# Performance work log

Measured on AMD Instinct MI355X. Metric: run time of the kernel, lower is better.

## Reference

```python
import jax, jax.numpy as jnp
import numpy as np

N, P, F, R, M = 20000, 320000, 128, 64, 32
F4 = F // 4            # n_atombasis // 4 == graph_n_messagebasis
L1 = 2                 # max_multipole_order + 1 (charges + dipoles)
N_BLOCKS = 2


def _w(key, fan_in, fan_out):
    return jax.random.normal(key, (fan_in, fan_out), dtype=jnp.float32) / np.sqrt(fan_in)


def setup_inputs() -> dict:
    key = jax.random.key(0)
    ks = jax.random.split(key, 24)
    inp = {
        'features': jax.random.normal(ks[0], (N, F), dtype=jnp.float32),
        'distances': jax.random.uniform(ks[1], (P,), dtype=jnp.float32),
        'vectors': jax.random.normal(ks[2], (P, 3), dtype=jnp.float32),
        'cutoffs': jax.random.uniform(ks[3], (P,), dtype=jnp.float32),
        'rbfs': jax.random.normal(ks[4], (P, R), dtype=jnp.float32),
        'idx_i': jnp.sort(jax.random.randint(ks[5], (P,), 0, N)),
        'idx_j': jax.random.randint(ks[6], (P,), 0, N),
    }
    d_inv = 6 * F4 + 2 * F   # (n_features_anisotropic+1)*(F//4) + 2*F = 448
    d_eq0 = F4 + 2 * F       # 288
    inp['Wrbf'] = _w(ks[7], R + 2 * F, F4)
    inp['Wemb'] = _w(ks[8], F, F)
    inp['eq0_W1'] = _w(ks[9], d_eq0, F)
    inp['eq0_b1'] = jnp.zeros((F,), jnp.float32)
    inp['eq0_W2'] = _w(ks[10], F, M * L1) * 0.01
    inp['eq1_W1'] = _w(ks[11], d_inv, F)
    inp['eq1_b1'] = jnp.zeros((F,), jnp.float32)
    inp['eq1_W2'] = _w(ks[12], F, M * L1) * 0.01
    inp['inv_W1'] = jnp.stack([_w(ks[13 + b], d_inv, F) for b in range(N_BLOCKS)])
    inp['inv_b1'] = jnp.zeros((N_BLOCKS, F), jnp.float32)
    inp['inv_W2'] = jnp.stack([_w(ks[15 + b], F, F) * 0.01 for b in range(N_BLOCKS)])
    inp['inv_b2'] = jnp.zeros((N_BLOCKS, F), jnp.float32)
    inp['upd_W1'] = jnp.stack([_w(ks[17 + b], 2 * F, F) for b in range(N_BLOCKS)])
    inp['upd_b1'] = jnp.zeros((N_BLOCKS, F), jnp.float32)
    inp['upd_W2'] = jnp.stack([_w(ks[19 + b], F, F) * 0.01 for b in range(N_BLOCKS)])
    inp['upd_b2'] = jnp.zeros((N_BLOCKS, F), jnp.float32)
    return inp


def reference(features, distances, vectors, cutoffs, rbfs, idx_i, idx_j,
              Wrbf, Wemb, eq0_W1, eq0_b1, eq0_W2, eq1_W1, eq1_b1, eq1_W2,
              inv_W1, inv_b1, inv_W2, inv_b2,
              upd_W1, upd_b1, upd_W2, upd_b2):
    silu = jax.nn.silu
    n_atoms = features.shape[0]
    # unit pair vectors (eps guards uniform distances near 0)
    u = vectors / (distances + 1e-3)[:, None]                 # [P,3]
    s = features                                              # [N,F] scalar features
    v = jnp.zeros((n_atoms, 3, M), dtype=features.dtype)      # [N,3,M] vector (dipole) features
    eq_params = [(eq0_W1, eq0_b1, eq0_W2), (eq1_W1, eq1_b1, eq1_W2)]
    for b in range(N_BLOCKS):
        si, sj = s[idx_i], s[idx_j]                           # gathers [P,F]
        e = jnp.concatenate([rbfs, si, sj], axis=-1) @ Wrbf   # pair embedding [P,F4]
        vi, vj = v[idx_i], v[idx_j]                           # [P,3,M]
        # anisotropic invariants of the equivariant features (5 of them, each [P,M])
        a_ui = jnp.einsum('pd,pdm->pm', u, vi)
        a_uj = jnp.einsum('pd,pdm->pm', u, vj)
        a_ij = jnp.sum(vi * vj, axis=1)
        a_ii = jnp.sum(vi * vi, axis=1)
        a_jj = jnp.sum(vj * vj, axis=1)
        x_inv = jnp.concatenate([e, a_ui, a_uj, a_ij, a_ii, a_jj, si, sj], axis=-1)  # [P,448]
        x_eq = jnp.concatenate([e, si, sj], axis=-1) if b == 0 else x_inv
        W1, b1, W2 = eq_params[b]
        g = silu(x_eq @ W1 + b1) @ W2                          # [P, M*2]
        g0, g1 = g[:, :M], g[:, M:]
        # equivariant message: radial direction term + propagated vector term
        dv = (g0[:, None, :] * u[:, :, None] + g1[:, None, :] * vj) * cutoffs[:, None, None]
        v = v + jax.ops.segment_sum(dv, idx_i, num_segments=n_atoms)
        # invariant message
        m = silu(silu(x_inv @ inv_W1[b] + inv_b1[b]) @ inv_W2[b] + inv_b2[b]) * cutoffs[:, None]
        s = s + jax.ops.segment_sum(m, idx_i, num_segments=n_atoms)
        # atom-wise update
        femb = s @ Wemb
        h = jnp.concatenate([s, femb], axis=-1)
        s = s + silu(silu(h @ upd_W1[b] + upd_b1[b]) @ upd_W2[b] + upd_b2[b])
    return s, v
```

## Files before the change

### kernel.cpp

```cpp
#include <hip/hip_runtime.h>
#include <math.h>

#define NA   20000
#define PE   320000
#define FDIM 128
#define ET   64
#define AT   32

typedef unsigned short ushort_t;
typedef __attribute__((ext_vector_type(8))) short bf16x8;
typedef __attribute__((ext_vector_type(4))) float f32x4;
#define MFMA16 __builtin_amdgcn_mfma_f32_16x16x32_bf16

#define XSTR     456
#define HSTR     136
#define XS_OFF   0
#define H1_OFF   58368
#define US_OFF   75776
#define IIS_OFF  76800
#define JJS_OFF  77064
#define SMEM_SZ  77320
#define ML_OFF   0
#define GL_OFF   33792

#define PK_W1EQ0   0
#define PK_W1EQ1   7168
#define PK_W1INV0  14336
#define PK_W1INV1  21504
#define PK_W2EQ0   28672
#define PK_W2EQ1   29696
#define PK_W2INV0  30720
#define PK_W2INV1  32768
#define PK_WRBF    34816
#define PK_WEMB    36096
#define PK_W1U0    38144
#define PK_W1U1    42240
#define PK_W2U0    46336
#define PK_W2U1    48384
#define PK_TOTAL   50432

__device__ __forceinline__ float silu_f(float z) {
    return z / (1.0f + __expf(-z));
}

__device__ __forceinline__ ushort_t f2bf(float x) {
    __bf16 h = (__bf16)x;
    union { __bf16 b; ushort_t u; } c; c.b = h; return c.u;
}

__device__ __forceinline__ unsigned int pack2bf(float x, float y) {
    return (unsigned int)f2bf(x) | ((unsigned int)f2bf(y) << 16);
}

__device__ __forceinline__ uint4 cvt8(float4 a, float4 b) {
    uint4 r;
    r.x = pack2bf(a.x, a.y); r.y = pack2bf(a.z, a.w);
    r.z = pack2bf(b.x, b.y); r.w = pack2bf(b.z, b.w);
    return r;
}

__global__ void pack_all(const float* __restrict__ eq0W1, const float* __restrict__ eq1W1,
                         const float* __restrict__ invW1, const float* __restrict__ eq0W2,
                         const float* __restrict__ eq1W2, const float* __restrict__ invW2,
                         const float* __restrict__ Wrbf,  const float* __restrict__ Wemb,
                         const float* __restrict__ updW1, const float* __restrict__ updW2,
                         ushort_t* __restrict__ out)
{
    const int tid = blockIdx.x * blockDim.x + threadIdx.x;
    if (tid >= PK_TOTAL) return;
    int base, KB, N, mode = 0;
    const float* src;
    if      (tid < PK_W1EQ1)  { base = PK_W1EQ0;  KB = 14; N = 128; src = eq0W1; mode = 1; }
    else if (tid < PK_W1INV0) { base = PK_W1EQ1;  KB = 14; N = 128; src = eq1W1; }
    else if (tid < PK_W1INV1) { base = PK_W1INV0; KB = 14; N = 128; src = invW1; }
    else if (tid < PK_W2EQ0)  { base = PK_W1INV1; KB = 14; N = 128; src = invW1 + 448 * 128; }
    else if (tid < PK_W2EQ1)  { base = PK_W2EQ0;  KB = 4;  N = 64;  src = eq0W2; }
    else if (tid < PK_W2INV0) { base = PK_W2EQ1;  KB = 4;  N = 64;  src = eq1W2; }
    else if (tid < PK_W2INV1) { base = PK_W2INV0; KB = 4;  N = 128; src = invW2; }
    else if (tid < PK_WRBF)   { base = PK_W2INV1; KB = 4;  N = 128; src = invW2 + 128 * 128; }
    else if (tid < PK_WEMB)   { base = PK_WRBF;   KB = 10; N = 32;  src = Wrbf; }
    else if (tid < PK_W1U0)   { base = PK_WEMB;   KB = 4;  N = 128; src = Wemb; }
    else if (tid < PK_W1U1)   { base = PK_W1U0;   KB = 8;  N = 128; src = updW1; }
    else if (tid < PK_W2U0)   { base = PK_W1U1;   KB = 8;  N = 128; src = updW1 + 256 * 128; }
    else if (tid < PK_W2U1)   { base = PK_W2U0;   KB = 4;  N = 128; src = updW2; }
    else                      { base = PK_W2U1;   KB = 4;  N = 128; src = updW2 + 128 * 128; }
    const int local = tid - base;
    const int lane  = local & 63;
    const int rest  = local >> 6;
    const int kb    = rest % KB;
    const int ct    = rest / KB;
    const int col   = ct * 16 + (lane & 15);
    const int k0    = kb * 32 + ((lane >> 4) * 8);
    ushort_t v[8];
    #pragma unroll
    for (int j = 0; j < 8; j++) {
        const int k = k0 + j;
        float x;
        if (mode == 1) x = (k < 32) ? src[k * N + col] : (k < 192 ? 0.f : src[(k - 160) * N + col]);
        else           x = src[(size_t)k * N + col];
        v[j] = f2bf(x);
    }
    *(uint4*)(out + (size_t)tid * 8) = *(uint4*)v;
}

__global__ __launch_bounds__(512, 4)
void edge_kernel(const float* __restrict__ rbfs,
                 const float* __restrict__ dists,
                 const float* __restrict__ vecs,
                 const float* __restrict__ cuts,
                 const int*   __restrict__ gidx_i,
                 const int*   __restrict__ gidx_j,
                 const ushort_t* __restrict__ s_bf,
                 const float* __restrict__ v_in,
                 const ushort_t* __restrict__ pWrbf,
                 const ushort_t* __restrict__ pW1eq,
                 const float* __restrict__ b1eq,
                 const ushort_t* __restrict__ pW2eq,
                 const ushort_t* __restrict__ pW1inv,
                 const float* __restrict__ b1inv,
                 const ushort_t* __restrict__ pW2inv,
                 const float* __restrict__ b2inv,
                 float* __restrict__ s_out,
                 float* __restrict__ v_out,
                 const int eqSkip)
{
    __shared__ __align__(16) char smem[SMEM_SZ];
    ushort_t* xs  = (ushort_t*)(smem + XS_OFF);
    ushort_t* h1  = (ushort_t*)(smem + H1_OFF);
    float*    us  = (float*)(smem + US_OFF);
    int*      iis = (int*)(smem + IIS_OFF);
    int*      jjs = (int*)(smem + JJS_OFF);
    float*    ml  = (float*)(smem + ML_OFF);
    float*    gl  = (float*)(smem + GL_OFF);

    const int t    = threadIdx.x;
    const int p0   = blockIdx.x * ET;
    const int lane = t & 63;
    const int wid  = t >> 6;
    const int colf = lane & 15;
    const int krow = (lane >> 4) * 8;

    {
        const int e = t >> 3, l = t & 7;
        const int p = p0 + e;
        const int i = gidx_i[p];
        const int j = gidx_j[p];
        const uint4* si4 = (const uint4*)(s_bf + (size_t)i * FDIM);
        const uint4* sj4 = (const uint4*)(s_bf + (size_t)j * FDIM);
        *(uint4*)&xs[e * XSTR + 192 + l * 16]     = si4[l * 2];
        *(uint4*)&xs[e * XSTR + 192 + l * 16 + 8] = si4[l * 2 + 1];
        *(uint4*)&xs[e * XSTR + 320 + l * 16]     = sj4[l * 2];
        *(uint4*)&xs[e * XSTR + 320 + l * 16 + 8] = sj4[l * 2 + 1];
        const float4* rb4 = (const float4*)(rbfs + (size_t)p * 64);
        float4 r0 = rb4[l * 2], r1 = rb4[l * 2 + 1];
        *(uint4*)&h1[e * HSTR + l * 8] = cvt8(r0, r1);
        if (t < ET) {
            const int pp = p0 + t;
            const float dinv = 1.0f / (dists[pp] + 0.001f);
            float4 uu;
            uu.x = vecs[pp * 3 + 0] * dinv;
            uu.y = vecs[pp * 3 + 1] * dinv;
            uu.z = vecs[pp * 3 + 2] * dinv;
            uu.w = cuts[pp];
            *(float4*)&us[t * 4] = uu;
            jjs[t] = gidx_j[pp];
        }
        if (t < ET + 1) {
            const int pp = p0 + t;
            iis[t] = (pp < PE) ? gidx_i[pp] : -1;
        }
    }
    __syncthreads();

    {
        const int e  = t >> 3;
        const int m0 = (t & 7) * 4;
        const int i = iis[e];
        const int j = jjs[e];
        float vi[3][4], vj[3][4];
        #pragma unroll
        for (int d = 0; d < 3; d++) {
            const float4 a = *(const float4*)(v_in + (size_t)i * 96 + d * 32 + m0);
            const float4 b = *(const float4*)(v_in + (size_t)j * 96 + d * 32 + m0);
            vi[d][0] = a.x; vi[d][1] = a.y; vi[d][2] = a.z; vi[d][3] = a.w;
            vj[d][0] = b.x; vj[d][1] = b.y; vj[d][2] = b.z; vj[d][3] = b.w;
        }
        const float ux = us[e * 4 + 0], uy = us[e * 4 + 1], uz = us[e * 4 + 2];
        float aui[4], auj[4], aij[4], aii[4], ajj[4];
        #pragma unroll
        for (int mm = 0; mm < 4; mm++) {
            aui[mm] = ux * vi[0][mm] + uy * vi[1][mm] + uz * vi[2][mm];
            auj[mm] = ux * vj[0][mm] + uy * vj[1][mm] + uz * vj[2][mm];
            aij[mm] = vi[0][mm] * vj[0][mm] + vi[1][mm] * vj[1][mm] + vi[2][mm] * vj[2][mm];
            aii[mm] = vi[0][mm] * vi[0][mm] + vi[1][mm] * vi[1][mm] + vi[2][mm] * vi[2][mm];
            ajj[mm] = vj[0][mm] * vj[0][mm] + vj[1][mm] * vj[1][mm] + vj[2][mm] * vj[2][mm];
        }
        uint2 w;
        w.x = pack2bf(aui[0], aui[1]); w.y = pack2bf(aui[2], aui[3]);
        *(uint2*)&xs[e * XSTR + 32 + m0] = w;
        w.x = pack2bf(auj[0], auj[1]); w.y = pack2bf(auj[2], auj[3]);
        *(uint2*)&xs[e * XSTR + 64 + m0] = w;
        w.x = pack2bf(aij[0], aij[1]); w.y = pack2bf(aij[2], aij[3]);
        *(uint2*)&xs[e * XSTR + 96 + m0] = w;
        w.x = pack2bf(aii[0], aii[1]); w.y = pack2bf(aii[2], aii[3]);
        *(uint2*)&xs[e * XSTR + 128 + m0] = w;
        w.x = pack2bf(ajj[0], ajj[1]); w.y = pack2bf(ajj[2], ajj[3]);
        *(uint2*)&xs[e * XSTR + 160 + m0] = w;
    }

    {
        const int rt = wid & 3;
        const int ct = wid >> 2;
        f32x4 eacc = {0.f, 0.f, 0.f, 0.f};
        #pragma unroll
        for (int kb = 0; kb < 10; kb++) {
            bf16x8 bf = *(const bf16x8*)(pWrbf + ((size_t)(ct * 10 + kb) * 64 + lane) * 8);
            bf16x8 af;
            if (kb < 2) af = *(const bf16x8*)&h1[(rt * 16 + colf) * HSTR + kb * 32 + krow];
            else        af = *(const bf16x8*)&xs[(rt * 16 + colf) * XSTR + 128 + kb * 32 + krow];
            eacc = MFMA16(af, bf, eacc, 0, 0, 0);
        }
        #pragma unroll
        for (int r = 0; r < 4; r++) {
            const int row = rt * 16 + (lane >> 4) * 4 + r;
            xs[row * XSTR + ct * 16 + colf] = f2bf(eacc[r]);
        }
    }
    __syncthreads();

    f32x4 ainv[4];
    {
        f32x4 aeq[4];
        const float bce = b1eq[wid * 16 + colf];
        const float bci = b1inv[wid * 16 + colf];
        #pragma unroll
        for (int rt = 0; rt < 4; rt++) {
            aeq[rt]  = (f32x4){bce, bce, bce, bce};
            ainv[rt] = (f32x4){bci, bci, bci, bci};
        }
        #pragma unroll
        for (int kb = 0; kb < 14; kb++) {
            bf16x8 af[4];
            #pragma unroll
            for (int rt = 0; rt < 4; rt++)
                af[rt] = *(const bf16x8*)&xs[(rt * 16 + colf) * XSTR + kb * 32 + krow];
            bf16x8 bi = *(const bf16x8*)(pW1inv + ((size_t)(wid * 14 + kb) * 64 + lane) * 8);
            #pragma unroll
            for (int rt = 0; rt < 4; rt++)
                ainv[rt] = MFMA16(af[rt], bi, ainv[rt], 0, 0, 0);
            if (!(eqSkip && kb >= 1 && kb < 6)) {
                bf16x8 be = *(const bf16x8*)(pW1eq + ((size_t)(wid * 14 + kb) * 64 + lane) * 8);
                #pragma unroll
                for (int rt = 0; rt < 4; rt++)
                    aeq[rt] = MFMA16(af[rt], be, aeq[rt], 0, 0, 0);
            }
        }
        #pragma unroll
        for (int rt = 0; rt < 4; rt++)
            #pragma unroll
            for (int r = 0; r < 4; r++) {
                const int row = rt * 16 + (lane >> 4) * 4 + r;
                h1[row * HSTR + wid * 16 + colf] = f2bf(silu_f(aeq[rt][r]));
            }
    }
    __syncthreads();

    f32x4 gacc[2];
    const int ct2 = wid & 3;
    const int rh  = wid >> 2;
    {
        gacc[0] = (f32x4){0.f, 0.f, 0.f, 0.f};
        gacc[1] = (f32x4){0.f, 0.f, 0.f, 0.f};
        #pragma unroll
        for (int kb = 0; kb < 4; kb++) {
            bf16x8 bf = *(const bf16x8*)(pW2eq + ((size_t)(ct2 * 4 + kb) * 64 + lane) * 8);
            #pragma unroll
            for (int q = 0; q < 2; q++) {
                bf16x8 af = *(const bf16x8*)&h1[((rh * 2 + q) * 16 + colf) * HSTR + kb * 32 + krow];
                gacc[q] = MFMA16(af, bf, gacc[q], 0, 0, 0);
            }
        }
    }
    __syncthreads();

    {
        #pragma unroll
        for (int rt = 0; rt < 4; rt++)
            #pragma unroll
            for (int r = 0; r < 4; r++) {
                const int row = rt * 16 + (lane >> 4) * 4 + r;
                h1[row * HSTR + wid * 16 + colf] = f2bf(silu_f(ainv[rt][r]));
            }
        #pragma unroll
        for (int q = 0; q < 2; q++)
            #pragma unroll
            for (int r = 0; r < 4; r++) {
                const int row = (rh * 2 + q) * 16 + (lane >> 4) * 4 + r;
                gl[row * 68 + ct2 * 16 + colf] = gacc[q][r];
            }
    }
    __syncthreads();

    {
        f32x4 macc[4];
        const float bc = b2inv[wid * 16 + colf];
        #pragma unroll
        for (int rt = 0; rt < 4; rt++) macc[rt] = (f32x4){bc, bc, bc, bc};
        #pragma unroll
        for (int kb = 0; kb < 4; kb++) {
            bf16x8 bf = *(const bf16x8*)(pW2inv + ((size_t)(wid * 4 + kb) * 64 + lane) * 8);
            #pragma unroll
            for (int rt = 0; rt < 4; rt++) {
                bf16x8 af = *(const bf16x8*)&h1[(rt * 16 + colf) * HSTR + kb * 32 + krow];
                macc[rt] = MFMA16(af, bf, macc[rt], 0, 0, 0);
            }
        }
        #pragma unroll
        for (int rt = 0; rt < 4; rt++)
            #pragma unroll
            for (int r = 0; r < 4; r++) {
                const int row = rt * 16 + (lane >> 4) * 4 + r;
                ml[row * 132 + wid * 16 + colf] = silu_f(macc[rt][r]) * us[row * 4 + 3];
            }
    }
    __syncthreads();

    {
        const int half = t >> 8;
        const int tl   = t & 255;
        if (tl < 224) {
            const int e0 = half * 32;
            if (tl < FDIM) {
                float acc = 0.f;
                for (int e = e0; e < e0 + 32; e++) {
                    acc += ml[e * 132 + tl];
                    if (e == e0 + 31 || iis[e + 1] != iis[e]) {
                        atomicAdd(&s_out[(size_t)iis[e] * FDIM + tl], acc);
                        acc = 0.f;
                    }
                }
            } else {
                const int col = tl - FDIM;
                const int d   = col >> 5;
                const int mm  = col & 31;
                float acc = 0.f;
                for (int e = e0; e < e0 + 32; e++) {
                    const float g0  = gl[e * 68 + mm];
                    const float g1  = gl[e * 68 + 32 + mm];
                    const float vjv = v_in[(size_t)jjs[e] * 96 + col];
                    acc = fmaf(us[e * 4 + 3], fmaf(g0, us[e * 4 + d], g1 * vjv), acc);
                    if (e == e0 + 31 || iis[e + 1] != iis[e]) {
                        atomicAdd(&v_out[(size_t)iis[e] * 96 + col], acc);
                        acc = 0.f;
                    }
                }
            }
        }
    }
}

__global__ __launch_bounds__(256, 4)
void node_kernel(const float* __restrict__ s_in,
                 const ushort_t* __restrict__ pWemb,
                 const ushort_t* __restrict__ pW1u,
                 const float* __restrict__ b1u,
                 const ushort_t* __restrict__ pW2u,
                 const float* __restrict__ b2u,
                 float* __restrict__ s_out,
                 ushort_t* __restrict__ sbf_out)
{
    __shared__ ushort_t ss[AT * HSTR];
    __shared__ ushort_t fe[AT * HSTR];
    __shared__ ushort_t t1[AT * HSTR];
    const int t    = threadIdx.x;
    const int a0   = blockIdx.x * AT;
    const int lane = t & 63;
    const int wid  = t >> 6;
    const int colf = lane & 15;
    const int krow = (lane >> 4) * 8;

    {
        const int a = t >> 3, l = t & 7;
        const float4* sr = (const float4*)(s_in + (size_t)(a0 + a) * FDIM);
        float4 q0 = sr[l * 4 + 0], q1 = sr[l * 4 + 1], q2 = sr[l * 4 + 2], q3 = sr[l * 4 + 3];
        *(uint4*)&ss[a * HSTR + l * 16]     = cvt8(q0, q1);
        *(uint4*)&ss[a * HSTR + l * 16 + 8] = cvt8(q2, q3);
    }
    __syncthreads();

    #pragma unroll
    for (int ci = 0; ci < 2; ci++) {
        const int ct = wid * 2 + ci;
        f32x4 acc[2];
        acc[0] = (f32x4){0.f, 0.f, 0.f, 0.f};
        acc[1] = (f32x4){0.f, 0.f, 0.f, 0.f};
        #pragma unroll
        for (int kb = 0; kb < 4; kb++) {
            bf16x8 bf = *(const bf16x8*)(pWemb + ((size_t)(ct * 4 + kb) * 64 + lane) * 8);
            #pragma unroll
            for (int rt = 0; rt < 2; rt++) {
                bf16x8 af = *(const bf16x8*)&ss[(rt * 16 + colf) * HSTR + kb * 32 + krow];
                acc[rt] = MFMA16(af, bf, acc[rt], 0, 0, 0);
            }
        }
        #pragma unroll
        for (int rt = 0; rt < 2; rt++)
            #pragma unroll
            for (int r = 0; r < 4; r++) {
                const int row = rt * 16 + (lane >> 4) * 4 + r;
                fe[row * HSTR + ct * 16 + colf] = f2bf(acc[rt][r]);
            }
    }
    __syncthreads();

    #pragma unroll
    for (int ci = 0; ci < 2; ci++) {
        const int ct = wid * 2 + ci;
        const float bc = b1u[ct * 16 + colf];
        f32x4 acc[2];
        acc[0] = (f32x4){bc, bc, bc, bc};
        acc[1] = (f32x4){bc, bc, bc, bc};
        #pragma unroll
        for (int kb = 0; kb < 8; kb++) {
            bf16x8 bf = *(const bf16x8*)(pW1u + ((size_t)(ct * 8 + kb) * 64 + lane) * 8);
            #pragma unroll
            for (int rt = 0; rt < 2; rt++) {
                bf16x8 af;
                if (kb < 4) af = *(const bf16x8*)&ss[(rt * 16 + colf) * HSTR + kb * 32 + krow];
                else        af = *(const bf16x8*)&fe[(rt * 16 + colf) * HSTR + (kb - 4) * 32 + krow];
                acc[rt] = MFMA16(af, bf, acc[rt], 0, 0, 0);
            }
        }
        #pragma unroll
        for (int rt = 0; rt < 2; rt++)
            #pragma unroll
            for (int r = 0; r < 4; r++) {
                const int row = rt * 16 + (lane >> 4) * 4 + r;
                t1[row * HSTR + ct * 16 + colf] = f2bf(silu_f(acc[rt][r]));
            }
    }
    __syncthreads();

    #pragma unroll
    for (int ci = 0; ci < 2; ci++) {
        const int ct = wid * 2 + ci;
        const float bc = b2u[ct * 16 + colf];
        f32x4 acc[2];
        acc[0] = (f32x4){bc, bc, bc, bc};
        acc[1] = (f32x4){bc, bc, bc, bc};
        #pragma unroll
        for (int kb = 0; kb < 4; kb++) {
            bf16x8 bf = *(const bf16x8*)(pW2u + ((size_t)(ct * 4 + kb) * 64 + lane) * 8);
            #pragma unroll
            for (int rt = 0; rt < 2; rt++) {
                bf16x8 af = *(const bf16x8*)&t1[(rt * 16 + colf) * HSTR + kb * 32 + krow];
                acc[rt] = MFMA16(af, bf, acc[rt], 0, 0, 0);
            }
        }
        #pragma unroll
        for (int rt = 0; rt < 2; rt++)
            #pragma unroll
            for (int r = 0; r < 4; r++) {
                const int row = rt * 16 + (lane >> 4) * 4 + r;
                const size_t off = (size_t)(a0 + row) * FDIM + ct * 16 + colf;
                const float o = s_in[off] + silu_f(acc[rt][r]);
                s_out[off] = o;
                sbf_out[off] = f2bf(o);
            }
    }
}

__global__ void copyf4(float4* __restrict__ dst, const float4* __restrict__ src, int n4) {
    int i = blockIdx.x * blockDim.x + threadIdx.x;
    const int stride = gridDim.x * blockDim.x;
    for (; i < n4; i += stride) dst[i] = src[i];
}

__global__ void zerof4(float4* __restrict__ dst, int n4) {
    int i = blockIdx.x * blockDim.x + threadIdx.x;
    const int stride = gridDim.x * blockDim.x;
    const float4 z = make_float4(0.f, 0.f, 0.f, 0.f);
    for (; i < n4; i += stride) dst[i] = z;
}

__global__ void cvt_bf(const float* __restrict__ in, ushort_t* __restrict__ out, int n8) {
    int i = blockIdx.x * blockDim.x + threadIdx.x;
    if (i < n8) {
        const float4* s = (const float4*)(in + (size_t)i * 8);
        *(uint4*)(out + (size_t)i * 8) = cvt8(s[0], s[1]);
    }
}

extern "C" void kernel_launch(void* const* d_in, const int* in_sizes, int n_in,
                              void* d_out, int out_size, void* d_ws, size_t ws_size,
                              hipStream_t stream) {
    (void)in_sizes; (void)n_in; (void)out_size; (void)ws_size;

    const float* features = (const float*)d_in[0];
    const float* dists    = (const float*)d_in[1];
    const float* vecs     = (const float*)d_in[2];
    const float* cuts     = (const float*)d_in[3];
    const float* rbfs     = (const float*)d_in[4];
    const int*   idx_i    = (const int*)d_in[5];
    const int*   idx_j    = (const int*)d_in[6];
    const float* Wrbf     = (const float*)d_in[7];
    const float* Wemb     = (const float*)d_in[8];
    const float* eq0_W1   = (const float*)d_in[9];
    const float* eq0_b1   = (const float*)d_in[10];
    const float* eq0_W2   = (const float*)d_in[11];
    const float* eq1_W1   = (const float*)d_in[12];
    const float* eq1_b1   = (const float*)d_in[13];
    const float* eq1_W2   = (const float*)d_in[14];
    const float* inv_W1   = (const float*)d_in[15];
    const float* inv_b1   = (const float*)d_in[16];
    const float* inv_W2   = (const float*)d_in[17];
    const float* inv_b2   = (const float*)d_in[18];
    const float* upd_W1   = (const float*)d_in[19];
    const float* upd_b1   = (const float*)d_in[20];
    const float* upd_W2   = (const float*)d_in[21];
    const float* upd_b2   = (const float*)d_in[22];

    float*    sA  = (float*)d_ws;
    float*    sB  = sA + (size_t)NA * FDIM;
    float*    vA  = sB + (size_t)NA * FDIM;
    float*    vB  = vA + (size_t)NA * 96;
    ushort_t* sbf = (ushort_t*)(vB + (size_t)NA * 96);
    ushort_t* pwb = sbf + (size_t)NA * FDIM;

    float* s_final = (float*)d_out;
    float* v_final = s_final + (size_t)NA * FDIM;

    const int SN4 = NA * FDIM / 4;
    const int VN4 = NA * 96 / 4;

    pack_all<<<(PK_TOTAL + 255) / 256, 256, 0, stream>>>(
        eq0_W1, eq1_W1, inv_W1, eq0_W2, eq1_W2, inv_W2, Wrbf, Wemb, upd_W1, upd_W2, pwb);
    cvt_bf<<<(NA * FDIM / 8 + 255) / 256, 256, 0, stream>>>(features, sbf, NA * FDIM / 8);
    copyf4<<<1024, 256, 0, stream>>>((float4*)sB, (const float4*)features, SN4);
    zerof4<<<1024, 256, 0, stream>>>((float4*)vA, VN4);
    zerof4<<<1024, 256, 0, stream>>>((float4*)vB, VN4);

    edge_kernel<<<PE / ET, 512, 0, stream>>>(
        rbfs, dists, vecs, cuts, idx_i, idx_j, sbf, vA,
        pwb + (size_t)PK_WRBF * 8,
        pwb + (size_t)PK_W1EQ0 * 8, eq0_b1, pwb + (size_t)PK_W2EQ0 * 8,
        pwb + (size_t)PK_W1INV0 * 8, inv_b1, pwb + (size_t)PK_W2INV0 * 8, inv_b2,
        sB, vB, 1);
    node_kernel<<<NA / AT, 256, 0, stream>>>(
        sB, pwb + (size_t)PK_WEMB * 8, pwb + (size_t)PK_W1U0 * 8, upd_b1,
        pwb + (size_t)PK_W2U0 * 8, upd_b2, sA, sbf);

    copyf4<<<1024, 256, 0, stream>>>((float4*)sB, (const float4*)sA, SN4);
    copyf4<<<1024, 256, 0, stream>>>((float4*)vA, (const float4*)vB, VN4);
    edge_kernel<<<PE / ET, 512, 0, stream>>>(
        rbfs, dists, vecs, cuts, idx_i, idx_j, sbf, vB,
        pwb + (size_t)PK_WRBF * 8,
        pwb + (size_t)PK_W1EQ1 * 8, eq1_b1, pwb + (size_t)PK_W2EQ1 * 8,
        pwb + (size_t)PK_W1INV1 * 8, inv_b1 + FDIM, pwb + (size_t)PK_W2INV1 * 8, inv_b2 + FDIM,
        sB, vA, 0);
    node_kernel<<<NA / AT, 256, 0, stream>>>(
        sB, pwb + (size_t)PK_WEMB * 8, pwb + (size_t)PK_W1U1 * 8, upd_b1 + FDIM,
        pwb + (size_t)PK_W2U1 * 8, upd_b2 + FDIM, s_final, sbf);

    copyf4<<<1024, 256, 0, stream>>>((float4*)v_final, (const float4*)vA, VN4);
}
```

Baseline: 653.9 us.

## Read si/sj MFMA operands from global, shrink LDS, drop redundant copies

The edge kernel no longer stages the gathered s_i/s_j rows in LDS. It reads the MFMA A-operands for those K-blocks directly from global (L2) through per-row pointers. This, plus storing the invariant message buffer as bf16, cuts shared memory from ~77KB to ~44KB so more blocks fit per CU, and the launch bounds are raised to 6. The host side removes intermediate copies by accumulating directly into sA and v_final. Risks: repeated global gathers per K-block, extra bf16 rounding of messages before summation, and register pressure from the higher occupancy target.

```diff
diff --git a/kernel.cpp b/kernel.cpp
--- a/kernel.cpp
+++ b/kernel.cpp
@@ -12,16 +12,16 @@
 typedef __attribute__((ext_vector_type(4))) float f32x4;
 #define MFMA16 __builtin_amdgcn_mfma_f32_16x16x32_bf16
 
-#define XSTR     456
+#define XSTR     200
 #define HSTR     136
 #define XS_OFF   0
-#define H1_OFF   58368
-#define US_OFF   75776
-#define IIS_OFF  76800
-#define JJS_OFF  77064
-#define SMEM_SZ  77320
-#define ML_OFF   0
-#define GL_OFF   33792
+#define H1_OFF   25600
+#define US_OFF   43008
+#define IIS_OFF  44032
+#define JJS_OFF  44292
+#define SMEM_SZ  44560
+#define GL_OFF   0
+#define ML_OFF   25600
 
 #define PK_W1EQ0   0
 #define PK_W1EQ1   7168
@@ -46,6 +46,10 @@
 __device__ __forceinline__ ushort_t f2bf(float x) {
     __bf16 h = (__bf16)x;
     union { __bf16 b; ushort_t u; } c; c.b = h; return c.u;
+}
+
+__device__ __forceinline__ float bf2f(ushort_t u) {
+    return __uint_as_float(((unsigned int)u) << 16);
 }
 
 __device__ __forceinline__ unsigned int pack2bf(float x, float y) {
@@ -103,7 +107,7 @@
     *(uint4*)(out + (size_t)tid * 8) = *(uint4*)v;
 }
 
-__global__ __launch_bounds__(512, 4)
+__global__ __launch_bounds__(512, 6)
 void edge_kernel(const float* __restrict__ rbfs,
                  const float* __restrict__ dists,
                  const float* __restrict__ vecs,
@@ -130,8 +134,8 @@
     float*    us  = (float*)(smem + US_OFF);
     int*      iis = (int*)(smem + IIS_OFF);
     int*      jjs = (int*)(smem + JJS_OFF);
-    float*    ml  = (float*)(smem + ML_OFF);
     float*    gl  = (float*)(smem + GL_OFF);
+    ushort_t* ml  = (ushort_t*)(smem + ML_OFF);
 
     const int t    = threadIdx.x;
     const int p0   = blockIdx.x * ET;
@@ -143,14 +147,6 @@
     {
         const int e = t >> 3, l = t & 7;
         const int p = p0 + e;
-        const int i = gidx_i[p];
-        const int j = gidx_j[p];
-        const uint4* si4 = (const uint4*)(s_bf + (size_t)i * FDIM);
-        const uint4* sj4 = (const uint4*)(s_bf + (size_t)j * FDIM);
-        *(uint4*)&xs[e * XSTR + 192 + l * 16]     = si4[l * 2];
-        *(uint4*)&xs[e * XSTR + 192 + l * 16 + 8] = si4[l * 2 + 1];
-        *(uint4*)&xs[e * XSTR + 320 + l * 16]     = sj4[l * 2];
-        *(uint4*)&xs[e * XSTR + 320 + l * 16 + 8] = sj4[l * 2 + 1];
         const float4* rb4 = (const float4*)(rbfs + (size_t)p * 64);
         float4 r0 = rb4[l * 2], r1 = rb4[l * 2 + 1];
         *(uint4*)&h1[e * HSTR + l * 8] = cvt8(r0, r1);
@@ -172,6 +168,14 @@
     }
     __syncthreads();
 
+    const ushort_t* siRow[4];
+    const ushort_t* sjRow[4];
+    #pragma unroll
+    for (int rt = 0; rt < 4; rt++) {
+        siRow[rt] = s_bf + (size_t)iis[rt * 16 + colf] * FDIM;
+        sjRow[rt] = s_bf + (size_t)jjs[rt * 16 + colf] * FDIM;
+    }
+
     {
         const int e  = t >> 3;
         const int m0 = (t & 7) * 4;
@@ -216,8 +220,9 @@
         for (int kb = 0; kb < 10; kb++) {
             bf16x8 bf = *(const bf16x8*)(pWrbf + ((size_t)(ct * 10 + kb) * 64 + lane) * 8);
             bf16x8 af;
-            if (kb < 2) af = *(const bf16x8*)&h1[(rt * 16 + colf) * HSTR + kb * 32 + krow];
-            else        af = *(const bf16x8*)&xs[(rt * 16 + colf) * XSTR + 128 + kb * 32 + krow];
+            if (kb < 2)      af = *(const bf16x8*)&h1[(rt * 16 + colf) * HSTR + kb * 32 + krow];
+            else if (kb < 6) af = *(const bf16x8*)(siRow[rt] + (kb - 2) * 32 + krow);
+            else             af = *(const bf16x8*)(sjRow[rt] + (kb - 6) * 32 + krow);
             eacc = MFMA16(af, bf, eacc, 0, 0, 0);
         }
         #pragma unroll
@@ -242,8 +247,11 @@
         for (int kb = 0; kb < 14; kb++) {
             bf16x8 af[4];
             #pragma unroll
-            for (int rt = 0; rt < 4; rt++)
-                af[rt] = *(const bf16x8*)&xs[(rt * 16 + colf) * XSTR + kb * 32 + krow];
+            for (int rt = 0; rt < 4; rt++) {
+                if (kb < 6)       af[rt] = *(const bf16x8*)&xs[(rt * 16 + colf) * XSTR + kb * 32 + krow];
+                else if (kb < 10) af[rt] = *(const bf16x8*)(siRow[rt] + (kb - 6) * 32 + krow);
+                else              af[rt] = *(const bf16x8*)(sjRow[rt] + (kb - 10) * 32 + krow);
+            }
             bf16x8 bi = *(const bf16x8*)(pW1inv + ((size_t)(wid * 14 + kb) * 64 + lane) * 8);
             #pragma unroll
             for (int rt = 0; rt < 4; rt++)
@@ -301,8 +309,8 @@
     }
     __syncthreads();
 
-    {
-        f32x4 macc[4];
+    f32x4 macc[4];
+    {
         const float bc = b2inv[wid * 16 + colf];
         #pragma unroll
         for (int rt = 0; rt < 4; rt++) macc[rt] = (f32x4){bc, bc, bc, bc};
@@ -315,12 +323,16 @@
                 macc[rt] = MFMA16(af, bf, macc[rt], 0, 0, 0);
             }
         }
+    }
+    __syncthreads();
+
+    {
         #pragma unroll
         for (int rt = 0; rt < 4; rt++)
             #pragma unroll
             for (int r = 0; r < 4; r++) {
                 const int row = rt * 16 + (lane >> 4) * 4 + r;
-                ml[row * 132 + wid * 16 + colf] = silu_f(macc[rt][r]) * us[row * 4 + 3];
+                ml[row * HSTR + wid * 16 + colf] = f2bf(silu_f(macc[rt][r]) * us[row * 4 + 3]);
             }
     }
     __syncthreads();
@@ -333,7 +345,7 @@
             if (tl < FDIM) {
                 float acc = 0.f;
                 for (int e = e0; e < e0 + 32; e++) {
-                    acc += ml[e * 132 + tl];
+                    acc += bf2f(ml[e * HSTR + tl]);
                     if (e == e0 + 31 || iis[e + 1] != iis[e]) {
                         atomicAdd(&s_out[(size_t)iis[e] * FDIM + tl], acc);
                         acc = 0.f;
@@ -359,7 +371,7 @@
     }
 }
 
-__global__ __launch_bounds__(256, 4)
+__global__ __launch_bounds__(256, 6)
 void node_kernel(const float* __restrict__ s_in,
                  const ushort_t* __restrict__ pWemb,
                  const ushort_t* __restrict__ pW1u,
@@ -550,17 +562,14 @@
         sB, pwb + (size_t)PK_WEMB * 8, pwb + (size_t)PK_W1U0 * 8, upd_b1,
         pwb + (size_t)PK_W2U0 * 8, upd_b2, sA, sbf);
 
-    copyf4<<<1024, 256, 0, stream>>>((float4*)sB, (const float4*)sA, SN4);
-    copyf4<<<1024, 256, 0, stream>>>((float4*)vA, (const float4*)vB, VN4);
+    copyf4<<<1024, 256, 0, stream>>>((float4*)v_final, (const float4*)vB, VN4);
     edge_kernel<<<PE / ET, 512, 0, stream>>>(
         rbfs, dists, vecs, cuts, idx_i, idx_j, sbf, vB,
         pwb + (size_t)PK_WRBF * 8,
         pwb + (size_t)PK_W1EQ1 * 8, eq1_b1, pwb + (size_t)PK_W2EQ1 * 8,
         pwb + (size_t)PK_W1INV1 * 8, inv_b1 + FDIM, pwb + (size_t)PK_W2INV1 * 8, inv_b2 + FDIM,
-        sB, vA, 0);
+        sA, v_final, 0);
     node_kernel<<<NA / AT, 256, 0, stream>>>(
-        sB, pwb + (size_t)PK_WEMB * 8, pwb + (size_t)PK_W1U1 * 8, upd_b1 + FDIM,
+        sA, pwb + (size_t)PK_WEMB * 8, pwb + (size_t)PK_W1U1 * 8, upd_b1 + FDIM,
         pwb + (size_t)PK_W2U1 * 8, upd_b2 + FDIM, s_final, sbf);
-
-    copyf4<<<1024, 256, 0, stream>>>((float4*)v_final, (const float4*)vA, VN4);
-}
+}
```

Measured after the change: 815.8 us. 24.8% more time.
